# Optimization experiments

Measured on AMD Instinct MI355X. Metric: run time of the kernel, lower is better.

Reference implementation:

```python
import jax, jax.numpy as jnp
import numpy as np

D_MODEL = 1024
N_HEADS = 16
HEAD_DIM = D_MODEL // N_HEADS
LN_EPS = 1e-6


def setup_inputs() -> dict:
    key = jax.random.key(0)
    ks = jax.random.split(key, 10)
    B, L, D = 4, 1024, D_MODEL
    s = 1.0 / np.sqrt(D)
    return {
        "q": jax.random.normal(ks[0], (B, L, D), jnp.float32),
        "k": jax.random.normal(ks[1], (B, L, D), jnp.float32),
        "v": jax.random.normal(ks[2], (B, L, D), jnp.float32),
        "masks": jnp.zeros((B, L, L), jnp.bool_),
        "Wq": jax.random.normal(ks[3], (D, D), jnp.float32) * s,
        "bq": jnp.zeros((D,), jnp.float32),
        "Wk": jax.random.normal(ks[4], (D, D), jnp.float32) * s,
        "bk": jnp.zeros((D,), jnp.float32),
        "Wv": jax.random.normal(ks[5], (D, D), jnp.float32) * s,
        "bv": jnp.zeros((D,), jnp.float32),
        "ln_g": jnp.ones((D,), jnp.float32),
        "ln_b": jnp.zeros((D,), jnp.float32),
    }


def _layer_norm(x, g, b):
    mu = jnp.mean(x, axis=-1, keepdims=True)
    var = jnp.var(x, axis=-1, keepdims=True)
    return (x - mu) * jax.lax.rsqrt(var + LN_EPS) * g + b


def reference(q, k, v, masks, Wq, bq, Wk, bk, Wv, bv, ln_g, ln_b):
    B, Lq, D = q.shape
    Lk = k.shape[1]
    H, Dh = N_HEADS, HEAD_DIM
    # linear projections (nn.Linear: x @ W.T + b)
    qp = q @ Wq.T + bq  # [B, Lq, D]
    kp = k @ Wk.T + bk
    vp = v @ Wv.T + bv
    # split heads: [B, L, D] -> [B, H, L, Dh]
    qh = qp.reshape(B, Lq, H, Dh).transpose(0, 2, 1, 3)
    kh = kp.reshape(B, Lk, H, Dh).transpose(0, 2, 1, 3)
    vh = vp.reshape(B, Lk, H, Dh).transpose(0, 2, 1, 3)
    scores = jnp.einsum("bhqd,bhkd->bhqk", qh, kh) / jnp.sqrt(jnp.float32(Dh))
    scores = jnp.where(masks[:, None, :, :], -jnp.inf, scores)
    attention = jax.nn.softmax(scores, axis=-1)  # [B, H, Lq, Lk]
    ctx = jnp.einsum("bhqk,bhkd->bhqd", attention, vh)  # [B, H, Lq, Dh]
    ctx = ctx.transpose(0, 2, 1, 3).reshape(B, Lq, D)  # unmulti_head
    output = _layer_norm(qp + ctx, ln_g, ln_b)  # residual is projected q
    return output, attention.reshape(B * H, Lq, Lk)
```

## Files before the change

### kernel.cpp

```cpp
#include <hip/hip_runtime.h>
#include <hip/hip_bf16.h>

typedef short bf16x8 __attribute__((ext_vector_type(8)));
typedef short bf16x4 __attribute__((ext_vector_type(4)));
typedef float f32x4 __attribute__((ext_vector_type(4)));
typedef unsigned short u16x8 __attribute__((ext_vector_type(8)));
typedef unsigned short u16x4 __attribute__((ext_vector_type(4)));

#define DEV static __device__ __forceinline__

DEV unsigned short f2bf(float f) {
  unsigned int u = __builtin_bit_cast(unsigned int, f);
  u += 0x7FFFu + ((u >> 16) & 1u);
  return (unsigned short)(u >> 16);
}
DEV float bf2f(unsigned short u) {
  return __builtin_bit_cast(float, (unsigned int)u << 16);
}

DEV void gload_lds16(const unsigned short* g, unsigned short* l) {
  __builtin_amdgcn_global_load_lds(
      (const __attribute__((address_space(1))) unsigned int*)g,
      (__attribute__((address_space(3))) unsigned int*)l, 16, 0, 0);
}

DEV void waitv(int n) {
  switch (n) {
    case 0: asm volatile("s_waitcnt vmcnt(0)" ::: "memory"); break;
    case 1: asm volatile("s_waitcnt vmcnt(1)" ::: "memory"); break;
    case 2: asm volatile("s_waitcnt vmcnt(2)" ::: "memory"); break;
    case 4: asm volatile("s_waitcnt vmcnt(4)" ::: "memory"); break;
    case 6: asm volatile("s_waitcnt vmcnt(6)" ::: "memory"); break;
    default: asm volatile("s_waitcnt vmcnt(0)" ::: "memory"); break;
  }
}

#define SB() __builtin_amdgcn_sched_barrier(0)
#define BAR() do { __builtin_amdgcn_s_barrier(); SB(); } while (0)
#define LBAR() do { asm volatile("s_waitcnt lgkmcnt(0)" ::: "memory"); \
                    SB(); \
                    __builtin_amdgcn_s_barrier(); \
                    SB(); } while (0)

__global__ __launch_bounds__(256) void cvt_kernel(
    const float* __restrict__ q, const float* __restrict__ k,
    const float* __restrict__ v, const float* __restrict__ wq,
    const float* __restrict__ wk, const float* __restrict__ wv,
    unsigned short* __restrict__ xq, unsigned short* __restrict__ xk,
    unsigned short* __restrict__ xv, unsigned short* __restrict__ wqb,
    unsigned short* __restrict__ wkb, unsigned short* __restrict__ wvb)
{
  int tid = blockIdx.x * 256 + threadIdx.x;
  const float* src; unsigned short* dst; int off;
  if      (tid <  524288) { src = q;  dst = xq;  off = tid; }
  else if (tid < 1048576) { src = k;  dst = xk;  off = tid -  524288; }
  else if (tid < 1572864) { src = v;  dst = xv;  off = tid - 1048576; }
  else if (tid < 1703936) { src = wq; dst = wqb; off = tid - 1572864; }
  else if (tid < 1835008) { src = wk; dst = wkb; off = tid - 1703936; }
  else                    { src = wv; dst = wvb; off = tid - 1835008; }
  size_t e = (size_t)off * 8;
  float4 a = *(const float4*)(src + e);
  float4 b = *(const float4*)(src + e + 4);
  u16x8 p = { f2bf(a.x), f2bf(a.y), f2bf(a.z), f2bf(a.w),
              f2bf(b.x), f2bf(b.y), f2bf(b.z), f2bf(b.w) };
  *(u16x8*)(dst + e) = p;
}

__global__ __launch_bounds__(512) void gemm_kernel(
    const unsigned short* __restrict__ xq, const unsigned short* __restrict__ xk,
    const unsigned short* __restrict__ xv, const unsigned short* __restrict__ wqb,
    const unsigned short* __restrict__ wkb, const unsigned short* __restrict__ wvb,
    const float* __restrict__ bq, const float* __restrict__ bk,
    const float* __restrict__ bv, unsigned short* __restrict__ qp,
    unsigned short* __restrict__ kp, unsigned short* __restrict__ vt)
{
  __shared__ union {
    struct { unsigned short A[128][64]; unsigned short B[128][64]; } ab;
    unsigned short T[128][128];
  } smu;
  const int t = threadIdx.x, lane = t & 63, wv8 = t >> 6;
  const int ln = lane & 15, g = lane >> 4;
  const int wm2 = wv8 >> 2, wn4 = wv8 & 3;
  const int seg = blockIdx.x >> 8, lb = blockIdx.x & 255;
  const int n0 = (lb & 7) * 128, m0 = (lb >> 3) * 128;

  const unsigned short* X; const unsigned short* W; const float* bias;
  unsigned short* outR; int mode;
  if (seg == 0)      { X = xq; W = wqb; bias = bq; outR = qp; mode = 0; }
  else if (seg == 1) { X = xk; W = wkb; bias = bk; outR = kp; mode = 0; }
  else               { X = xv; W = wvb; bias = bv; outR = vt; mode = 2; }

  f32x4 acc[4][2];
#pragma unroll
  for (int i = 0; i < 4; ++i)
#pragma unroll
    for (int j = 0; j < 2; ++j) acc[i][j] = {0.f, 0.f, 0.f, 0.f};

  const int lrow = lane >> 3, lcol = (lane & 7) * 8;
  for (int kt = 0; kt < 16; ++kt) {
    const int k0 = kt * 64;
    __syncthreads();
#pragma unroll
    for (int i = 0; i < 2; ++i) {
      const int r = wv8 * 16 + i * 8;
      gload_lds16(X + (size_t)(m0 + r + lrow) * 1024 + k0 + lcol, &smu.ab.A[r][0]);
      gload_lds16(W + (size_t)(n0 + r + lrow) * 1024 + k0 + lcol, &smu.ab.B[r][0]);
    }
    __syncthreads();
#pragma unroll
    for (int ks = 0; ks < 2; ++ks) {
      bf16x8 af[4], bfr[2];
#pragma unroll
      for (int i = 0; i < 4; ++i)
        af[i] = *(const bf16x8*)&smu.ab.A[wm2 * 64 + i * 16 + ln][ks * 32 + g * 8];
#pragma unroll
      for (int j = 0; j < 2; ++j)
        bfr[j] = *(const bf16x8*)&smu.ab.B[wn4 * 32 + j * 16 + ln][ks * 32 + g * 8];
#pragma unroll
      for (int i = 0; i < 4; ++i)
#pragma unroll
        for (int j = 0; j < 2; ++j)
          acc[i][j] = __builtin_amdgcn_mfma_f32_16x16x32_bf16(
              af[i], bfr[j], acc[i][j], 0, 0, 0);
    }
  }

  float bvv[2];
#pragma unroll
  for (int j = 0; j < 2; ++j) bvv[j] = bias[n0 + wn4 * 32 + j * 16 + ln];

  if (mode == 0) {
#pragma unroll
    for (int i = 0; i < 4; ++i)
#pragma unroll
      for (int j = 0; j < 2; ++j)
#pragma unroll
        for (int r = 0; r < 4; ++r) {
          int row = m0 + wm2 * 64 + i * 16 + g * 4 + r;
          int col = n0 + wn4 * 32 + j * 16 + ln;
          outR[(size_t)row * 1024 + col] = f2bf(acc[i][j][r] + bvv[j]);
        }
  } else {
    __syncthreads();
#pragma unroll
    for (int i = 0; i < 4; ++i)
#pragma unroll
      for (int j = 0; j < 2; ++j)
#pragma unroll
        for (int r = 0; r < 4; ++r)
          smu.T[wn4 * 32 + j * 16 + ln][wm2 * 64 + i * 16 + g * 4 + r] =
              f2bf(acc[i][j][r] + bvv[j]);
    __syncthreads();
    const int bb = m0 >> 10, l0 = m0 & 1023;
#pragma unroll
    for (int it = 0; it < 4; ++it) {
      const int col = it * 32 + (t >> 4);
      const int r8 = (t & 15) * 8;
      *(u16x8*)&outR[((size_t)(bb * 16 + (n0 >> 6) + (col >> 6)) * 64 + (col & 63)) * 1024 + l0 + r8] =
          *(const u16x8*)&smu.T[col][r8];
    }
  }
}

__global__ __launch_bounds__(512, 2) void attn_kernel(
    const unsigned short* __restrict__ qp, const unsigned short* __restrict__ kp,
    const unsigned short* __restrict__ vt, const unsigned char* __restrict__ masks,
    float* __restrict__ attn_out, float* __restrict__ res_out)
{
  __shared__ union {
    unsigned short Kw[8][3][1024];
    unsigned short Vb[3][64][128];
    float ctxp[4][32][68];
  } sm;
  __shared__ float red[2][2][16][4];

  const int t = threadIdx.x;
  const int wv = t >> 6, lane = t & 63;
  const int ln = lane & 15, g = lane >> 4;
  const int wq = wv & 3, wm = wv >> 2;
  const int hw = blockIdx.x;
  const int lid = (hw & 7) * 256 + (hw >> 3);
  const int b = lid >> 9, h = (lid >> 5) & 15, m0 = (lid & 31) * 32;
  const size_t rowbase = (size_t)(b * 1024 + m0);

  bf16x8 qf[2];
  {
    const unsigned short* qb =
        qp + (rowbase + wm * 16 + ln) * 1024 + h * 64 + g * 8;
    qf[0] = *(const bf16x8*)qb;
    qf[1] = *(const bf16x8*)(qb + 32);
  }
  SB();

  const int slr8 = lane >> 3;
  const int suK = (lane & 7) ^ slr8;
  const int vlr = lane >> 4;
  const int vu1 = (lane & 15) ^ vlr;
  const int vu2 = (lane & 15) ^ (4 + vlr);
  const unsigned short* kbase = kp + (size_t)b * 1048576 + h * 64;
  const unsigned short* vtb = vt + ((size_t)(b * 16 + h) * 64) * 1024;
  unsigned short* kwv = &sm.Kw[wv][0][0];

#define STAGE_K(tt) do { \
    gload_lds16(kbase + (size_t)((tt) * 64 + wq * 16 + slr8) * 1024 + suK * 8, \
                kwv + ((tt) % 3) * 1024); \
    gload_lds16(kbase + (size_t)((tt) * 64 + wq * 16 + 8 + slr8) * 1024 + suK * 8, \
                kwv + ((tt) % 3) * 1024 + 512); } while (0)
#define STAGE_V(c) do { \
    gload_lds16(vtb + (size_t)(wv * 8 + vlr) * 1024 + (c) * 128 + vu1 * 8, \
                &sm.Vb[(c) % 3][wv * 8][0]); \
    gload_lds16(vtb + (size_t)(wv * 8 + 4 + vlr) * 1024 + (c) * 128 + vu2 * 8, \
                &sm.Vb[(c) % 3][wv * 8 + 4][0]); } while (0)

  f32x4 sc[16];
#pragma unroll
  for (int i = 0; i < 16; ++i) sc[i] = {0.f, 0.f, 0.f, 0.f};

  STAGE_K(0); STAGE_K(1);
  SB();
#pragma unroll
  for (int tt = 0; tt < 16; ++tt) {
    waitv(tt <= 14 ? 2 : 0);
    SB();
    if (tt + 2 < 16) STAGE_K(tt + 2);
    SB();
    const unsigned short* ksl = kwv + (tt % 3) * 1024 + ln * 64;
    bf16x8 kf0 = *(const bf16x8*)(ksl + (g ^ (ln & 7)) * 8);
    bf16x8 kf1 = *(const bf16x8*)(ksl + ((4 + g) ^ (ln & 7)) * 8);
    sc[tt] = __builtin_amdgcn_mfma_f32_16x16x32_bf16(kf0, qf[0], sc[tt], 0, 0, 0);
    sc[tt] = __builtin_amdgcn_mfma_f32_16x16x32_bf16(kf1, qf[1], sc[tt], 0, 0, 0);
  }

  unsigned mw[16];
  {
    const unsigned char* mrow =
        masks + ((size_t)b * 1024 + m0 + wm * 16 + ln) * 1024 + wq * 16 + g * 4;
#pragma unroll
    for (int tt = 0; tt < 16; ++tt) mw[tt] = *(const unsigned*)(mrow + tt * 64);
  }
  SB();

  LBAR();
  STAGE_V(0); STAGE_V(1);
  SB();

  const float C = 0.18033688011112042f;
  float mx = -3.0e30f;
#pragma unroll
  for (int tt = 0; tt < 16; ++tt) {
    if (mw[tt]) {
#pragma unroll
      for (int r = 0; r < 4; ++r)
        if ((mw[tt] >> (8 * r)) & 0xffu) sc[tt][r] = -1.0e30f;
    }
#pragma unroll
    for (int r = 0; r < 4; ++r) mx = fmaxf(mx, sc[tt][r]);
  }
  mx = fmaxf(mx, __shfl_xor(mx, 16));
  mx = fmaxf(mx, __shfl_xor(mx, 32));
  if (g == 0) red[0][wm][ln][wq] = mx;
  LBAR();
  mx = fmaxf(fmaxf(red[0][wm][ln][0], red[0][wm][ln][1]),
             fmaxf(red[0][wm][ln][2], red[0][wm][ln][3]));
  const float mt = mx * C;

  float sum = 0.f;
#pragma unroll
  for (int tt = 0; tt < 16; ++tt)
#pragma unroll
    for (int r = 0; r < 4; ++r) {
      float p = exp2f(__builtin_fmaf(sc[tt][r], C, -mt));
      sc[tt][r] = p;
      sum += p;
    }
  sum += __shfl_xor(sum, 16);
  sum += __shfl_xor(sum, 32);
  if (g == 0) red[1][wm][ln][wq] = sum;
  LBAR();
  float l4 = red[1][wm][ln][0] + red[1][wm][ln][1] +
             red[1][wm][ln][2] + red[1][wm][ln][3];
  float rinv = 1.0f / l4;

  bf16x8 af8[8];
#pragma unroll
  for (int c = 0; c < 8; ++c) {
    bf16x8 a;
#pragma unroll
    for (int r = 0; r < 4; ++r) a[r]     = (short)f2bf(sc[2 * c][r] * rinv);
#pragma unroll
    for (int r = 0; r < 4; ++r) a[4 + r] = (short)f2bf(sc[2 * c + 1][r] * rinv);
    af8[c] = a;
  }

  f32x4 cacc[4];
#pragma unroll
  for (int i = 0; i < 4; ++i) cacc[i] = {0.f, 0.f, 0.f, 0.f};
  const size_t abase =
      ((size_t)(b * 16 + h) * 1024 + (m0 + wm * 16 + ln)) * 1024 + wq * 16 + g * 4;
#pragma unroll
  for (int c = 0; c < 8; ++c) {
    waitv(c == 0 ? 2 : (c == 1 ? 4 : (c <= 6 ? 6 : 4)));
    BAR();
    if (c + 2 < 8) STAGE_V(c + 2);
    SB();
#pragma unroll
    for (int ni = 0; ni < 4; ++ni) {
      const int d = ni * 16 + ln;
      const int u0 = (2 * wq + (g >> 1)) ^ (ln & 7);
      const int u1 = (8 + 2 * wq + (g >> 1)) ^ (ln & 7);
      bf16x4 b0 = *(const bf16x4*)&sm.Vb[c % 3][d][u0 * 8 + (g & 1) * 4];
      bf16x4 b1 = *(const bf16x4*)&sm.Vb[c % 3][d][u1 * 8 + (g & 1) * 4];
      bf16x8 bfr = { b0[0], b0[1], b0[2], b0[3], b1[0], b1[1], b1[2], b1[3] };
      cacc[ni] = __builtin_amdgcn_mfma_f32_16x16x32_bf16(af8[c], bfr, cacc[ni], 0, 0, 0);
    }
    SB();
#pragma unroll
    for (int hf = 0; hf < 2; ++hf) {
      f32x4 v = { bf2f((unsigned short)af8[c][hf * 4 + 0]),
                  bf2f((unsigned short)af8[c][hf * 4 + 1]),
                  bf2f((unsigned short)af8[c][hf * 4 + 2]),
                  bf2f((unsigned short)af8[c][hf * 4 + 3]) };
      *(f32x4*)(attn_out + abase + (2 * c + hf) * 64) = v;
    }
    SB();
  }

  LBAR();
#pragma unroll
  for (int ni = 0; ni < 4; ++ni)
#pragma unroll
    for (int r = 0; r < 4; ++r)
      sm.ctxp[wq][wm * 16 + g * 4 + r][ni * 16 + ln] = cacc[ni][r];
  LBAR();
  {
    const int m = t >> 4, d4 = (t & 15) * 4;
    f32x4 s0 = *(const f32x4*)&sm.ctxp[0][m][d4];
    f32x4 s1 = *(const f32x4*)&sm.ctxp[1][m][d4];
    f32x4 s2 = *(const f32x4*)&sm.ctxp[2][m][d4];
    f32x4 s3 = *(const f32x4*)&sm.ctxp[3][m][d4];
    f32x4 s = s0 + s1 + s2 + s3;
    const unsigned short* qrow = qp + (rowbase + m) * 1024 + h * 64 + d4;
    u16x4 qv = *(const u16x4*)qrow;
    f32x4 qf32 = { bf2f(qv[0]), bf2f(qv[1]), bf2f(qv[2]), bf2f(qv[3]) };
    s = s + qf32;
    *(f32x4*)(res_out + (rowbase + m) * 1024 + h * 64 + d4) = s;
  }
#undef STAGE_K
#undef STAGE_V
}

__global__ __launch_bounds__(256) void ln_kernel(
    float* __restrict__ io,
    const float* __restrict__ gma, const float* __restrict__ bta)
{
  __shared__ float rbuf[2][4];
  const int r = blockIdx.x, t = threadIdx.x;
  const int i4 = t * 4;
  const size_t base = (size_t)r * 1024 + i4;
  f32x4 x = *(const f32x4*)(io + base);
  float s = x[0] + x[1] + x[2] + x[3];
  float q = x[0]*x[0] + x[1]*x[1] + x[2]*x[2] + x[3]*x[3];
#pragma unroll
  for (int off = 1; off < 64; off <<= 1) {
    s += __shfl_xor(s, off);
    q += __shfl_xor(q, off);
  }
  const int wv = t >> 6;
  if ((t & 63) == 0) { rbuf[0][wv] = s; rbuf[1][wv] = q; }
  __syncthreads();
  s = rbuf[0][0] + rbuf[0][1] + rbuf[0][2] + rbuf[0][3];
  q = rbuf[1][0] + rbuf[1][1] + rbuf[1][2] + rbuf[1][3];
  float mu = s * (1.0f / 1024.0f);
  float var = q * (1.0f / 1024.0f) - mu * mu;
  float is = rsqrtf(var + 1e-6f);
  f32x4 gv = *(const f32x4*)(gma + i4);
  f32x4 bv = *(const f32x4*)(bta + i4);
  f32x4 o;
#pragma unroll
  for (int k = 0; k < 4; ++k) o[k] = (x[k] - mu) * is * gv[k] + bv[k];
  *(f32x4*)(io + base) = o;
}

extern "C" void kernel_launch(void* const* d_in, const int* in_sizes, int n_in,
                              void* d_out, int out_size, void* d_ws, size_t ws_size,
                              hipStream_t stream) {
  const float* q  = (const float*)d_in[0];
  const float* k  = (const float*)d_in[1];
  const float* v  = (const float*)d_in[2];
  const unsigned char* masks = (const unsigned char*)d_in[3];
  const float* Wq = (const float*)d_in[4];
  const float* bq = (const float*)d_in[5];
  const float* Wk = (const float*)d_in[6];
  const float* bk = (const float*)d_in[7];
  const float* Wv = (const float*)d_in[8];
  const float* bv = (const float*)d_in[9];
  const float* lg = (const float*)d_in[10];
  const float* lb = (const float*)d_in[11];

  float* out = (float*)d_out;
  float* attn_out = out + (size_t)4 * 1024 * 1024;

  unsigned short* xq  = (unsigned short*)attn_out;
  unsigned short* xk  = xq + 4194304;
  unsigned short* xv  = xk + 4194304;
  unsigned short* wqb = xv + 4194304;
  unsigned short* wkb = wqb + 1048576;
  unsigned short* wvb = wkb + 1048576;

  unsigned short* qp = (unsigned short*)d_ws;
  unsigned short* kp = qp + 4194304;
  unsigned short* vt = kp + 4194304;

  hipLaunchKernelGGL(cvt_kernel, dim3(7680), dim3(256), 0, stream,
                     q, k, v, Wq, Wk, Wv, xq, xk, xv, wqb, wkb, wvb);
  hipLaunchKernelGGL(gemm_kernel, dim3(768), dim3(512), 0, stream,
                     xq, xk, xv, wqb, wkb, wvb, bq, bk, bv, qp, kp, vt);
  hipLaunchKernelGGL(attn_kernel, dim3(2048), dim3(512), 0, stream,
                     qp, kp, vt, masks, attn_out, out);
  hipLaunchKernelGGL(ln_kernel, dim3(4096), dim3(256), 0, stream,
                     out, lg, lb);
}
```

Measured before the change: 193.9 us.

## Fuse fp32-to-bf16 conversion into GEMM, single-pass softmax merge, MFMA priority

Removes the separate conversion kernel: the projection GEMM now loads fp32 inputs and weights directly, converts them to bf16 in registers and writes swizzled LDS tiles. The block-to-tile mapping is reordered, and the transpose buffer is padded. In attention, the two cross-wave reductions (max, then sum) become one, using per-wave local max/sum combined with rescaling, and probabilities are recomputed via exp2 with a folded log-normaliser instead of multiplying by a reciprocal. s_setprio is raised around MFMA blocks. The trade-off is that the GEMM loses async global-to-LDS loads and reads twice the bytes per tile, with extra exp2 work in softmax.

```diff
diff --git a/kernel.cpp b/kernel.cpp
--- a/kernel.cpp
+++ b/kernel.cpp
@@ -41,54 +41,34 @@
                     SB(); \
                     __builtin_amdgcn_s_barrier(); \
                     SB(); } while (0)
-
-__global__ __launch_bounds__(256) void cvt_kernel(
-    const float* __restrict__ q, const float* __restrict__ k,
-    const float* __restrict__ v, const float* __restrict__ wq,
-    const float* __restrict__ wk, const float* __restrict__ wv,
-    unsigned short* __restrict__ xq, unsigned short* __restrict__ xk,
-    unsigned short* __restrict__ xv, unsigned short* __restrict__ wqb,
-    unsigned short* __restrict__ wkb, unsigned short* __restrict__ wvb)
-{
-  int tid = blockIdx.x * 256 + threadIdx.x;
-  const float* src; unsigned short* dst; int off;
-  if      (tid <  524288) { src = q;  dst = xq;  off = tid; }
-  else if (tid < 1048576) { src = k;  dst = xk;  off = tid -  524288; }
-  else if (tid < 1572864) { src = v;  dst = xv;  off = tid - 1048576; }
-  else if (tid < 1703936) { src = wq; dst = wqb; off = tid - 1572864; }
-  else if (tid < 1835008) { src = wk; dst = wkb; off = tid - 1703936; }
-  else                    { src = wv; dst = wvb; off = tid - 1835008; }
-  size_t e = (size_t)off * 8;
-  float4 a = *(const float4*)(src + e);
-  float4 b = *(const float4*)(src + e + 4);
-  u16x8 p = { f2bf(a.x), f2bf(a.y), f2bf(a.z), f2bf(a.w),
-              f2bf(b.x), f2bf(b.y), f2bf(b.z), f2bf(b.w) };
-  *(u16x8*)(dst + e) = p;
-}
+#define PRIO1() __builtin_amdgcn_s_setprio(1)
+#define PRIO0() __builtin_amdgcn_s_setprio(0)
 
 __global__ __launch_bounds__(512) void gemm_kernel(
-    const unsigned short* __restrict__ xq, const unsigned short* __restrict__ xk,
-    const unsigned short* __restrict__ xv, const unsigned short* __restrict__ wqb,
-    const unsigned short* __restrict__ wkb, const unsigned short* __restrict__ wvb,
+    const float* __restrict__ xq, const float* __restrict__ xk,
+    const float* __restrict__ xv, const float* __restrict__ wqf,
+    const float* __restrict__ wkf, const float* __restrict__ wvf,
     const float* __restrict__ bq, const float* __restrict__ bk,
     const float* __restrict__ bv, unsigned short* __restrict__ qp,
     unsigned short* __restrict__ kp, unsigned short* __restrict__ vt)
 {
   __shared__ union {
     struct { unsigned short A[128][64]; unsigned short B[128][64]; } ab;
-    unsigned short T[128][128];
+    unsigned short T[128][132];
   } smu;
   const int t = threadIdx.x, lane = t & 63, wv8 = t >> 6;
   const int ln = lane & 15, g = lane >> 4;
   const int wm2 = wv8 >> 2, wn4 = wv8 & 3;
   const int seg = blockIdx.x >> 8, lb = blockIdx.x & 255;
-  const int n0 = (lb & 7) * 128, m0 = (lb >> 3) * 128;
-
-  const unsigned short* X; const unsigned short* W; const float* bias;
+  const int x8 = lb & 7, s32 = lb >> 3;
+  const int m0 = (x8 * 4 + (s32 >> 3)) * 128;
+  const int n0 = (s32 & 7) * 128;
+
+  const float* X; const float* W; const float* bias;
   unsigned short* outR; int mode;
-  if (seg == 0)      { X = xq; W = wqb; bias = bq; outR = qp; mode = 0; }
-  else if (seg == 1) { X = xk; W = wkb; bias = bk; outR = kp; mode = 0; }
-  else               { X = xv; W = wvb; bias = bv; outR = vt; mode = 2; }
+  if (seg == 0)      { X = xq; W = wqf; bias = bq; outR = qp; mode = 0; }
+  else if (seg == 1) { X = xk; W = wkf; bias = bk; outR = kp; mode = 0; }
+  else               { X = xv; W = wvf; bias = bv; outR = vt; mode = 2; }
 
   f32x4 acc[4][2];
 #pragma unroll
@@ -96,32 +76,55 @@
 #pragma unroll
     for (int j = 0; j < 2; ++j) acc[i][j] = {0.f, 0.f, 0.f, 0.f};
 
-  const int lrow = lane >> 3, lcol = (lane & 7) * 8;
+  const int srow = t >> 2;
+  const int su0 = (t & 3) * 2;
+  const int swz = srow & 7;
   for (int kt = 0; kt < 16; ++kt) {
     const int k0 = kt * 64;
     __syncthreads();
-#pragma unroll
-    for (int i = 0; i < 2; ++i) {
-      const int r = wv8 * 16 + i * 8;
-      gload_lds16(X + (size_t)(m0 + r + lrow) * 1024 + k0 + lcol, &smu.ab.A[r][0]);
-      gload_lds16(W + (size_t)(n0 + r + lrow) * 1024 + k0 + lcol, &smu.ab.B[r][0]);
+    {
+      const float* ga = X + (size_t)(m0 + srow) * 1024 + k0 + su0 * 8;
+      float4 a0 = *(const float4*)ga;
+      float4 a1 = *(const float4*)(ga + 4);
+      float4 a2 = *(const float4*)(ga + 8);
+      float4 a3 = *(const float4*)(ga + 12);
+      u16x8 p0 = { f2bf(a0.x), f2bf(a0.y), f2bf(a0.z), f2bf(a0.w),
+                   f2bf(a1.x), f2bf(a1.y), f2bf(a1.z), f2bf(a1.w) };
+      u16x8 p1 = { f2bf(a2.x), f2bf(a2.y), f2bf(a2.z), f2bf(a2.w),
+                   f2bf(a3.x), f2bf(a3.y), f2bf(a3.z), f2bf(a3.w) };
+      *(u16x8*)&smu.ab.A[srow][(su0 ^ swz) * 8] = p0;
+      *(u16x8*)&smu.ab.A[srow][((su0 + 1) ^ swz) * 8] = p1;
+      const float* gb = W + (size_t)(n0 + srow) * 1024 + k0 + su0 * 8;
+      float4 b0 = *(const float4*)gb;
+      float4 b1 = *(const float4*)(gb + 4);
+      float4 b2 = *(const float4*)(gb + 8);
+      float4 b3 = *(const float4*)(gb + 12);
+      u16x8 q0 = { f2bf(b0.x), f2bf(b0.y), f2bf(b0.z), f2bf(b0.w),
+                   f2bf(b1.x), f2bf(b1.y), f2bf(b1.z), f2bf(b1.w) };
+      u16x8 q1 = { f2bf(b2.x), f2bf(b2.y), f2bf(b2.z), f2bf(b2.w),
+                   f2bf(b3.x), f2bf(b3.y), f2bf(b3.z), f2bf(b3.w) };
+      *(u16x8*)&smu.ab.B[srow][(su0 ^ swz) * 8] = q0;
+      *(u16x8*)&smu.ab.B[srow][((su0 + 1) ^ swz) * 8] = q1;
     }
     __syncthreads();
 #pragma unroll
     for (int ks = 0; ks < 2; ++ks) {
       bf16x8 af[4], bfr[2];
+      const int ru = (ks * 4 + g) ^ (ln & 7);
 #pragma unroll
       for (int i = 0; i < 4; ++i)
-        af[i] = *(const bf16x8*)&smu.ab.A[wm2 * 64 + i * 16 + ln][ks * 32 + g * 8];
+        af[i] = *(const bf16x8*)&smu.ab.A[wm2 * 64 + i * 16 + ln][ru * 8];
 #pragma unroll
       for (int j = 0; j < 2; ++j)
-        bfr[j] = *(const bf16x8*)&smu.ab.B[wn4 * 32 + j * 16 + ln][ks * 32 + g * 8];
+        bfr[j] = *(const bf16x8*)&smu.ab.B[wn4 * 32 + j * 16 + ln][ru * 8];
+      PRIO1();
 #pragma unroll
       for (int i = 0; i < 4; ++i)
 #pragma unroll
         for (int j = 0; j < 2; ++j)
           acc[i][j] = __builtin_amdgcn_mfma_f32_16x16x32_bf16(
               af[i], bfr[j], acc[i][j], 0, 0, 0);
+      PRIO0();
     }
   }
 
@@ -227,8 +230,10 @@
     const unsigned short* ksl = kwv + (tt % 3) * 1024 + ln * 64;
     bf16x8 kf0 = *(const bf16x8*)(ksl + (g ^ (ln & 7)) * 8);
     bf16x8 kf1 = *(const bf16x8*)(ksl + ((4 + g) ^ (ln & 7)) * 8);
+    PRIO1();
     sc[tt] = __builtin_amdgcn_mfma_f32_16x16x32_bf16(kf0, qf[0], sc[tt], 0, 0, 0);
     sc[tt] = __builtin_amdgcn_mfma_f32_16x16x32_bf16(kf1, qf[1], sc[tt], 0, 0, 0);
+    PRIO0();
   }
 
   unsigned mw[16];
@@ -258,37 +263,35 @@
   }
   mx = fmaxf(mx, __shfl_xor(mx, 16));
   mx = fmaxf(mx, __shfl_xor(mx, 32));
-  if (g == 0) red[0][wm][ln][wq] = mx;
-  LBAR();
-  mx = fmaxf(fmaxf(red[0][wm][ln][0], red[0][wm][ln][1]),
-             fmaxf(red[0][wm][ln][2], red[0][wm][ln][3]));
-  const float mt = mx * C;
-
+  const float mtl = mx * C;
   float sum = 0.f;
 #pragma unroll
   for (int tt = 0; tt < 16; ++tt)
 #pragma unroll
-    for (int r = 0; r < 4; ++r) {
-      float p = exp2f(__builtin_fmaf(sc[tt][r], C, -mt));
-      sc[tt][r] = p;
-      sum += p;
-    }
+    for (int r = 0; r < 4; ++r)
+      sum += exp2f(__builtin_fmaf(sc[tt][r], C, -mtl));
   sum += __shfl_xor(sum, 16);
   sum += __shfl_xor(sum, 32);
-  if (g == 0) red[1][wm][ln][wq] = sum;
+  if (g == 0) { red[0][wm][ln][wq] = mx; red[1][wm][ln][wq] = sum; }
   LBAR();
-  float l4 = red[1][wm][ln][0] + red[1][wm][ln][1] +
-             red[1][wm][ln][2] + red[1][wm][ln][3];
-  float rinv = 1.0f / l4;
+  float m4 = fmaxf(fmaxf(red[0][wm][ln][0], red[0][wm][ln][1]),
+                   fmaxf(red[0][wm][ln][2], red[0][wm][ln][3]));
+  float l4 = 0.f;
+#pragma unroll
+  for (int i = 0; i < 4; ++i)
+    l4 += red[1][wm][ln][i] * exp2f((red[0][wm][ln][i] - m4) * C);
+  const float beta = __builtin_fmaf(-m4, C, -__builtin_log2f(l4));
 
   bf16x8 af8[8];
 #pragma unroll
   for (int c = 0; c < 8; ++c) {
     bf16x8 a;
 #pragma unroll
-    for (int r = 0; r < 4; ++r) a[r]     = (short)f2bf(sc[2 * c][r] * rinv);
-#pragma unroll
-    for (int r = 0; r < 4; ++r) a[4 + r] = (short)f2bf(sc[2 * c + 1][r] * rinv);
+    for (int r = 0; r < 4; ++r)
+      a[r] = (short)f2bf(exp2f(__builtin_fmaf(sc[2 * c][r], C, beta)));
+#pragma unroll
+    for (int r = 0; r < 4; ++r)
+      a[4 + r] = (short)f2bf(exp2f(__builtin_fmaf(sc[2 * c + 1][r], C, beta)));
     af8[c] = a;
   }
 
@@ -311,7 +314,9 @@
       bf16x4 b0 = *(const bf16x4*)&sm.Vb[c % 3][d][u0 * 8 + (g & 1) * 4];
       bf16x4 b1 = *(const bf16x4*)&sm.Vb[c % 3][d][u1 * 8 + (g & 1) * 4];
       bf16x8 bfr = { b0[0], b0[1], b0[2], b0[3], b1[0], b1[1], b1[2], b1[3] };
+      PRIO1();
       cacc[ni] = __builtin_amdgcn_mfma_f32_16x16x32_bf16(af8[c], bfr, cacc[ni], 0, 0, 0);
+      PRIO0();
     }
     SB();
 #pragma unroll
@@ -400,21 +405,12 @@
   float* out = (float*)d_out;
   float* attn_out = out + (size_t)4 * 1024 * 1024;
 
-  unsigned short* xq  = (unsigned short*)attn_out;
-  unsigned short* xk  = xq + 4194304;
-  unsigned short* xv  = xk + 4194304;
-  unsigned short* wqb = xv + 4194304;
-  unsigned short* wkb = wqb + 1048576;
-  unsigned short* wvb = wkb + 1048576;
-
   unsigned short* qp = (unsigned short*)d_ws;
   unsigned short* kp = qp + 4194304;
   unsigned short* vt = kp + 4194304;
 
-  hipLaunchKernelGGL(cvt_kernel, dim3(7680), dim3(256), 0, stream,
-                     q, k, v, Wq, Wk, Wv, xq, xk, xv, wqb, wkb, wvb);
   hipLaunchKernelGGL(gemm_kernel, dim3(768), dim3(512), 0, stream,
-                     xq, xk, xv, wqb, wkb, wvb, bq, bk, bv, qp, kp, vt);
+                     q, k, v, Wq, Wk, Wv, bq, bk, bv, qp, kp, vt);
   hipLaunchKernelGGL(attn_kernel, dim3(2048), dim3(512), 0, stream,
                      qp, kp, vt, masks, attn_out, out);
   hipLaunchKernelGGL(ln_kernel, dim3(4096), dim3(256), 0, stream,
```

Result: slower. 206.3 us (+6.4%).

## Double-buffer projection GEMM, swizzle LDS, fuse softmax reductions, add MFMA priority

Applied to the files above, without the earlier changes.

The projection GEMM moves to double-buffered LDS with an XOR-swizzled column layout, one barrier per k-step, a remapped block-to-tile order, padded transpose storage and a two-blocks-per-CU launch bound. The attention softmax replaces its two cross-wave barriers (max then sum) with one: each wave computes a local max and sum, and the combined result is rescaled into a single log-domain offset that is applied as exp2 when building probabilities. s_setprio is raised around MFMA groups in both kernels. The aim is to cut LDS bank conflicts, barrier stalls and load latency, at the cost of recomputing exp2 twice per score.

```diff
diff --git a/kernel.cpp b/kernel.cpp
--- a/kernel.cpp
+++ b/kernel.cpp
@@ -41,6 +41,8 @@
                     SB(); \
                     __builtin_amdgcn_s_barrier(); \
                     SB(); } while (0)
+#define PRIO1() __builtin_amdgcn_s_setprio(1)
+#define PRIO0() __builtin_amdgcn_s_setprio(0)
 
 __global__ __launch_bounds__(256) void cvt_kernel(
     const float* __restrict__ q, const float* __restrict__ k,
@@ -66,7 +68,7 @@
   *(u16x8*)(dst + e) = p;
 }
 
-__global__ __launch_bounds__(512) void gemm_kernel(
+__global__ __launch_bounds__(512, 2) void gemm_kernel(
     const unsigned short* __restrict__ xq, const unsigned short* __restrict__ xk,
     const unsigned short* __restrict__ xv, const unsigned short* __restrict__ wqb,
     const unsigned short* __restrict__ wkb, const unsigned short* __restrict__ wvb,
@@ -75,14 +77,16 @@
     unsigned short* __restrict__ kp, unsigned short* __restrict__ vt)
 {
   __shared__ union {
-    struct { unsigned short A[128][64]; unsigned short B[128][64]; } ab;
-    unsigned short T[128][128];
+    unsigned short ab[2][2][128][64];
+    unsigned short T[128][132];
   } smu;
   const int t = threadIdx.x, lane = t & 63, wv8 = t >> 6;
   const int ln = lane & 15, g = lane >> 4;
   const int wm2 = wv8 >> 2, wn4 = wv8 & 3;
   const int seg = blockIdx.x >> 8, lb = blockIdx.x & 255;
-  const int n0 = (lb & 7) * 128, m0 = (lb >> 3) * 128;
+  const int x8 = lb & 7, s32 = lb >> 3;
+  const int m0 = (x8 * 4 + (s32 >> 3)) * 128;
+  const int n0 = (s32 & 7) * 128;
 
   const unsigned short* X; const unsigned short* W; const float* bias;
   unsigned short* outR; int mode;
@@ -96,33 +100,49 @@
 #pragma unroll
     for (int j = 0; j < 2; ++j) acc[i][j] = {0.f, 0.f, 0.f, 0.f};
 
-  const int lrow = lane >> 3, lcol = (lane & 7) * 8;
+  const int lrow = lane >> 3;
+  const int lcol = ((lane & 7) ^ lrow) * 8;
+
+#define STAGE_G(kt) do { \
+    const int _k0 = (kt) * 64; \
+    _Pragma("unroll") \
+    for (int i = 0; i < 2; ++i) { \
+      const int r = wv8 * 16 + i * 8; \
+      gload_lds16(X + (size_t)(m0 + r + lrow) * 1024 + _k0 + lcol, \
+                  &smu.ab[(kt) & 1][0][r][0]); \
+      gload_lds16(W + (size_t)(n0 + r + lrow) * 1024 + _k0 + lcol, \
+                  &smu.ab[(kt) & 1][1][r][0]); \
+    } } while (0)
+
+  STAGE_G(0);
+  waitv(0);
+  BAR();
+#pragma unroll 2
   for (int kt = 0; kt < 16; ++kt) {
-    const int k0 = kt * 64;
-    __syncthreads();
-#pragma unroll
-    for (int i = 0; i < 2; ++i) {
-      const int r = wv8 * 16 + i * 8;
-      gload_lds16(X + (size_t)(m0 + r + lrow) * 1024 + k0 + lcol, &smu.ab.A[r][0]);
-      gload_lds16(W + (size_t)(n0 + r + lrow) * 1024 + k0 + lcol, &smu.ab.B[r][0]);
-    }
-    __syncthreads();
+    if (kt < 15) STAGE_G(kt + 1);
+    SB();
 #pragma unroll
     for (int ks = 0; ks < 2; ++ks) {
       bf16x8 af[4], bfr[2];
+      const int ru = ((ks * 4 + g) ^ (ln & 7)) * 8;
 #pragma unroll
       for (int i = 0; i < 4; ++i)
-        af[i] = *(const bf16x8*)&smu.ab.A[wm2 * 64 + i * 16 + ln][ks * 32 + g * 8];
+        af[i] = *(const bf16x8*)&smu.ab[kt & 1][0][wm2 * 64 + i * 16 + ln][ru];
 #pragma unroll
       for (int j = 0; j < 2; ++j)
-        bfr[j] = *(const bf16x8*)&smu.ab.B[wn4 * 32 + j * 16 + ln][ks * 32 + g * 8];
+        bfr[j] = *(const bf16x8*)&smu.ab[kt & 1][1][wn4 * 32 + j * 16 + ln][ru];
+      PRIO1();
 #pragma unroll
       for (int i = 0; i < 4; ++i)
 #pragma unroll
         for (int j = 0; j < 2; ++j)
           acc[i][j] = __builtin_amdgcn_mfma_f32_16x16x32_bf16(
               af[i], bfr[j], acc[i][j], 0, 0, 0);
+      PRIO0();
     }
+    SB();
+    waitv(0);
+    BAR();
   }
 
   float bvv[2];
@@ -160,6 +180,7 @@
           *(const u16x8*)&smu.T[col][r8];
     }
   }
+#undef STAGE_G
 }
 
 __global__ __launch_bounds__(512, 2) void attn_kernel(
@@ -227,8 +248,10 @@
     const unsigned short* ksl = kwv + (tt % 3) * 1024 + ln * 64;
     bf16x8 kf0 = *(const bf16x8*)(ksl + (g ^ (ln & 7)) * 8);
     bf16x8 kf1 = *(const bf16x8*)(ksl + ((4 + g) ^ (ln & 7)) * 8);
+    PRIO1();
     sc[tt] = __builtin_amdgcn_mfma_f32_16x16x32_bf16(kf0, qf[0], sc[tt], 0, 0, 0);
     sc[tt] = __builtin_amdgcn_mfma_f32_16x16x32_bf16(kf1, qf[1], sc[tt], 0, 0, 0);
+    PRIO0();
   }
 
   unsigned mw[16];
@@ -258,37 +281,35 @@
   }
   mx = fmaxf(mx, __shfl_xor(mx, 16));
   mx = fmaxf(mx, __shfl_xor(mx, 32));
-  if (g == 0) red[0][wm][ln][wq] = mx;
-  LBAR();
-  mx = fmaxf(fmaxf(red[0][wm][ln][0], red[0][wm][ln][1]),
-             fmaxf(red[0][wm][ln][2], red[0][wm][ln][3]));
-  const float mt = mx * C;
-
+  const float mtl = mx * C;
   float sum = 0.f;
 #pragma unroll
   for (int tt = 0; tt < 16; ++tt)
 #pragma unroll
-    for (int r = 0; r < 4; ++r) {
-      float p = exp2f(__builtin_fmaf(sc[tt][r], C, -mt));
-      sc[tt][r] = p;
-      sum += p;
-    }
+    for (int r = 0; r < 4; ++r)
+      sum += exp2f(__builtin_fmaf(sc[tt][r], C, -mtl));
   sum += __shfl_xor(sum, 16);
   sum += __shfl_xor(sum, 32);
-  if (g == 0) red[1][wm][ln][wq] = sum;
+  if (g == 0) { red[0][wm][ln][wq] = mx; red[1][wm][ln][wq] = sum; }
   LBAR();
-  float l4 = red[1][wm][ln][0] + red[1][wm][ln][1] +
-             red[1][wm][ln][2] + red[1][wm][ln][3];
-  float rinv = 1.0f / l4;
+  float m4 = fmaxf(fmaxf(red[0][wm][ln][0], red[0][wm][ln][1]),
+                   fmaxf(red[0][wm][ln][2], red[0][wm][ln][3]));
+  float l4 = 0.f;
+#pragma unroll
+  for (int i = 0; i < 4; ++i)
+    l4 += red[1][wm][ln][i] * exp2f((red[0][wm][ln][i] - m4) * C);
+  const float beta = __builtin_fmaf(-m4, C, -__builtin_log2f(l4));
 
   bf16x8 af8[8];
 #pragma unroll
   for (int c = 0; c < 8; ++c) {
     bf16x8 a;
 #pragma unroll
-    for (int r = 0; r < 4; ++r) a[r]     = (short)f2bf(sc[2 * c][r] * rinv);
-#pragma unroll
-    for (int r = 0; r < 4; ++r) a[4 + r] = (short)f2bf(sc[2 * c + 1][r] * rinv);
+    for (int r = 0; r < 4; ++r)
+      a[r] = (short)f2bf(exp2f(__builtin_fmaf(sc[2 * c][r], C, beta)));
+#pragma unroll
+    for (int r = 0; r < 4; ++r)
+      a[4 + r] = (short)f2bf(exp2f(__builtin_fmaf(sc[2 * c + 1][r], C, beta)));
     af8[c] = a;
   }
 
@@ -311,7 +332,9 @@
       bf16x4 b0 = *(const bf16x4*)&sm.Vb[c % 3][d][u0 * 8 + (g & 1) * 4];
       bf16x4 b1 = *(const bf16x4*)&sm.Vb[c % 3][d][u1 * 8 + (g & 1) * 4];
       bf16x8 bfr = { b0[0], b0[1], b0[2], b0[3], b1[0], b1[1], b1[2], b1[3] };
+      PRIO1();
       cacc[ni] = __builtin_amdgcn_mfma_f32_16x16x32_bf16(af8[c], bfr, cacc[ni], 0, 0, 0);
+      PRIO0();
     }
     SB();
 #pragma unroll
```

Result: faster. 177.3 us (-8.6%).
